# Performance work log

Hardware: AMD Instinct MI355X
Metric: run time of the kernel (lower is better)

## Reference

```python
import jax, jax.numpy as jnp
import numpy as np

B, S, D, H = 512, 256, 512, 512  # batch, seq_len, input_size, hidden_size (D==H required by module math)


def setup_inputs() -> dict:
    key = jax.random.key(0)
    ks = jax.random.split(key, 16)
    stdv = 1.0 / np.sqrt(H)
    u = lambda k, shp: jax.random.uniform(k, shp, jnp.float32, -stdv, stdv)
    return {
        "x": jax.random.normal(ks[0], (B, S, D), jnp.float32),
        "time_sen_seqs": jax.random.uniform(ks[1], (B, S), jnp.float32),  # attenuation rates in [0,1)
        "W_e": u(ks[2], (D, H)), "b_e": u(ks[3], (H,)),
        "U_i": u(ks[4], (D, H)), "V_i": u(ks[5], (H, H)), "b_i": u(ks[6], (H,)),
        "U_f": u(ks[7], (D, H)), "V_f": u(ks[8], (H, H)), "b_f": u(ks[9], (H,)),
        "U_c": u(ks[10], (D, H)), "V_c": u(ks[11], (H, H)), "b_c": u(ks[12], (H,)),
        "U_o": u(ks[13], (D, H)), "V_o": u(ks[14], (H, H)), "b_o": u(ks[15], (H,)),
    }


def reference(x, time_sen_seqs, W_e, b_e, U_i, V_i, b_i, U_f, V_f, b_f,
              U_c, V_c, b_c, U_o, V_o, b_o):
    bs = x.shape[0]
    h0 = jnp.zeros((bs, H), x.dtype)
    c0 = jnp.zeros((bs, H), x.dtype)

    # Precompute all input projections in one batched GEMM: [S, B, 4H]
    U = jnp.concatenate([U_i, U_f, U_c, U_o], axis=1)           # [D, 4H]
    b = jnp.concatenate([b_i, b_f, b_c, b_o], axis=0)           # [4H]
    x_proj = jnp.einsum('bsd,dk->sbk', x, U) + b                # [S, B, 4H]
    forget_seq = time_sen_seqs.T[..., None]                     # [S, B, 1]

    def step(carry, inp):
        h, c = carry
        xp, f_att = inp
        xi, xf, xc, xo = jnp.split(xp, 4, axis=-1)
        i_t = jax.nn.sigmoid(xi + h @ V_i)
        f_t = jax.nn.sigmoid(xf + h @ V_f)
        g_t = jnp.tanh(xc + h @ V_c)
        o_t = jax.nn.sigmoid(xo + h @ V_o)
        c = jnp.tanh((c * f_att) @ W_e + b_e)   # sentiment attenuation transform
        c = f_t * c + i_t * g_t
        h = o_t * jnp.tanh(c)
        return (h, c), h

    (h_t, c_t), hs = jax.lax.scan(step, (h0, c0), (x_proj, forget_seq))
    hidden_seq = hs.transpose(1, 0, 2)          # [B, S, H]
    return hidden_seq, (h_t, c_t)
```

## Files before the change

kernel.cpp:

```cpp
#include <hip/hip_runtime.h>

#define B_SZ 512
#define S_SZ 256
#define D_SZ 512
#define H_SZ 512

typedef __bf16 bf16x8 __attribute__((ext_vector_type(8)));
typedef __bf16 bf16x4 __attribute__((ext_vector_type(4)));
typedef float f32x4 __attribute__((ext_vector_type(4)));
typedef int i32x4 __attribute__((ext_vector_type(4)));
typedef unsigned long long u64;

#define FLAGS_BYTES 65536
#define STATE_OFF FLAGS_BYTES
#define STATE_PAR_ELEMS (2 * H_SZ * B_SZ)
#define GWT_OFF_BYTES (STATE_OFF + 2097152)
#define WET_OFF_BYTES (GWT_OFF_BYTES + 4194304)
#define XB_OFF_BYTES (WET_OFF_BYTES + 524288)
#define XB_BYTES ((size_t)B_SZ * S_SZ * D_SZ * 2)

#define SWZ(j, k) ((k) ^ (((j) & 7) << 3) ^ ((((j) >> 3) & 1) << 6))

__device__ __forceinline__ float sigmoidf_(float v) {
    return 1.f / (1.f + __expf(-v));
}
__device__ __forceinline__ float tanhf_(float v) {
    return 1.f - 2.f / (1.f + __expf(2.f * v));
}

__device__ __forceinline__ u64 coh_load(const u64* p) {
    return __hip_atomic_load(p, __ATOMIC_RELAXED, __HIP_MEMORY_SCOPE_AGENT);
}
__device__ __forceinline__ void coh_store(u64* p, u64 v) {
    __hip_atomic_store(p, v, __ATOMIC_RELAXED, __HIP_MEMORY_SCOPE_AGENT);
}

__global__ __launch_bounds__(256) void prep_weights(
    const float* __restrict__ We,
    const float* __restrict__ Ui, const float* __restrict__ Vi,
    const float* __restrict__ Uf, const float* __restrict__ Vf,
    const float* __restrict__ Uc, const float* __restrict__ Vc,
    const float* __restrict__ Uo, const float* __restrict__ Vo,
    __bf16* __restrict__ GwT, __bf16* __restrict__ WeT)
{
    const int bid = blockIdx.x;
    const int tid = threadIdx.x;
    if (bid < 2048) {
        const int g = bid >> 9;
        const int j = bid & 511;
        const float* U = (g == 0) ? Ui : (g == 1) ? Uf : (g == 2) ? Uc : Uo;
        const float* V = (g == 0) ? Vi : (g == 1) ? Vf : (g == 2) ? Vc : Vo;
        __bf16* dst = GwT + ((size_t)(g * 512 + j) << 10);
        for (int k = tid; k < 1024; k += 256) {
            float v = (k < 512) ? U[k * 512 + j] : V[(k - 512) * 512 + j];
            dst[k] = (__bf16)v;
        }
    } else {
        const int j = bid - 2048;
        __bf16* dst = WeT + ((size_t)j << 9);
        for (int k = tid; k < 512; k += 256) {
            dst[k] = (__bf16)We[k * 512 + j];
        }
    }
}

__global__ __launch_bounds__(256) void xcvt(const float* __restrict__ x,
                                            __bf16* __restrict__ xb)
{
    const size_t i = ((size_t)blockIdx.x * 256 + threadIdx.x) * 8;
    f32x4 a = *(const f32x4*)(x + i);
    f32x4 b = *(const f32x4*)(x + i + 4);
    bf16x8 o;
    o[0] = (__bf16)a[0]; o[1] = (__bf16)a[1]; o[2] = (__bf16)a[2]; o[3] = (__bf16)a[3];
    o[4] = (__bf16)b[0]; o[5] = (__bf16)b[1]; o[6] = (__bf16)b[2]; o[7] = (__bf16)b[3];
    *(bf16x8*)(xb + i) = o;
}

template <bool XB>
__global__ __launch_bounds__(256, 1) void lstm_persist(
    const float* __restrict__ x, const __bf16* __restrict__ xb,
    const float* __restrict__ tseq,
    const float* __restrict__ b_i, const float* __restrict__ b_f,
    const float* __restrict__ b_c, const float* __restrict__ b_o,
    const float* __restrict__ b_e,
    const __bf16* __restrict__ GwT, const __bf16* __restrict__ WeT,
    __bf16* __restrict__ state, int* __restrict__ flags,
    float* __restrict__ out)
{
    __shared__ __align__(16) __bf16 wlds[4][16][1024];
    __shared__ __align__(16) __bf16 welds[16][512];

    const int tid = threadIdx.x;
    const int bid = blockIdx.x;
    const int rblk = bid & 7;
    const int cblk = bid >> 3;
    const int j0 = cblk << 4;
    const int wave = tid >> 6;
    const int lane = tid & 63;
    const int alr = lane & 15;
    const int hq = lane >> 4;
    const int kbase = hq * 8;

    for (int e = tid * 8; e < 4 * 16 * 1024; e += 256 * 8) {
        const int g = e >> 14;
        const int j = (e >> 10) & 15;
        const int k = e & 1023;
        *(uint4*)&wlds[g][j][SWZ(j, k)] =
            *(const uint4*)&GwT[((size_t)(g * 512 + j0 + j) << 10) + k];
    }
    for (int e = tid * 8; e < 16 * 512; e += 256 * 8) {
        const int j = e >> 9;
        const int k = e & 511;
        *(uint4*)&welds[j][SWZ(j, k)] =
            *(const uint4*)&WeT[((size_t)(j0 + j) << 9) + k];
    }
    __syncthreads();

    bf16x8 wxr[8][4];
    #pragma unroll
    for (int kk = 0; kk < 8; ++kk)
        #pragma unroll
        for (int g = 0; g < 4; ++g)
            wxr[kk][g] = *(const bf16x8*)&wlds[g][alr][SWZ(alr, kk * 32 + kbase)];

    const int brow = rblk * 64 + wave * 16 + alr;
    const int jbase = j0 + hq * 4;
    const f32x4 Bi4 = *(const f32x4*)(b_i + jbase);
    const f32x4 Bf4 = *(const f32x4*)(b_f + jbase);
    const f32x4 Bc4 = *(const f32x4*)(b_c + jbase);
    const f32x4 Bo4 = *(const f32x4*)(b_o + jbase);
    const f32x4 Be4 = *(const f32x4*)(b_e + jbase);

    const float* xrow = x + (size_t)brow * S_SZ * D_SZ;
    const __bf16* xrowb = XB ? xb + (size_t)brow * S_SZ * D_SZ : nullptr;
    const float* tsrow = tseq + (size_t)brow * S_SZ;
    const size_t hoff = (size_t)brow * H_SZ;
    float* outrow = out + (size_t)brow * S_SZ * H_SZ + jbase;

    int* gflags = flags + rblk * 32 * 32;
    int* myflag = gflags + cblk * 32;
    const int* pollp = gflags + (lane & 31) * 32;

    int* xgrp = flags + 8192 + rblk * 32 * 32;
    unsigned xcc;
    asm volatile("s_getreg_b32 %0, hwreg(HW_REG_XCC_ID)" : "=s"(xcc));
    if (tid == 0)
        __hip_atomic_store(xgrp + cblk * 32, (int)xcc + 1,
                           __ATOMIC_RELAXED, __HIP_MEMORY_SCOPE_AGENT);
    int vx;
    const int* xpoll = xgrp + (lane & 31) * 32;
    for (;;) {
        vx = __hip_atomic_load(xpoll, __ATOMIC_RELAXED, __HIP_MEMORY_SCOPE_AGENT);
        if (__all(vx != 0)) break;
        __builtin_amdgcn_s_sleep(1);
    }
    const bool l2ok = __all(vx == __shfl(vx, 0, 64));

    bf16x8 xbf[16];
    if constexpr (XB) {
        #pragma unroll
        for (int kk = 0; kk < 16; ++kk)
            xbf[kk] = *(const bf16x8*)(xrowb + kk * 32 + kbase);
    } else {
        f32x4 xf0[32];
        #pragma unroll
        for (int kk = 0; kk < 16; ++kk) {
            xf0[2 * kk]     = *(const f32x4*)(xrow + kk * 32 + kbase);
            xf0[2 * kk + 1] = *(const f32x4*)(xrow + kk * 32 + kbase + 4);
        }
        #pragma unroll
        for (int kk = 0; kk < 16; ++kk) {
            f32x4 u = xf0[2 * kk], v = xf0[2 * kk + 1];
            bf16x8 a;
            a[0] = (__bf16)u[0]; a[1] = (__bf16)u[1]; a[2] = (__bf16)u[2]; a[3] = (__bf16)u[3];
            a[4] = (__bf16)v[0]; a[5] = (__bf16)v[1]; a[6] = (__bf16)v[2]; a[7] = (__bf16)v[3];
            xbf[kk] = a;
        }
    }

    for (int t = 0; t < S_SZ; ++t) {
        const __bf16* hp = state + (size_t)(t & 1) * STATE_PAR_ELEMS;
        const __bf16* cp = hp + (size_t)H_SZ * B_SZ;
        __bf16* hnx = state + (size_t)((t + 1) & 1) * STATE_PAR_ELEMS;
        __bf16* cnx = hnx + (size_t)H_SZ * B_SZ;

        const float fa = (t + 1 < S_SZ) ? tsrow[t + 1] : 0.f;
        union HU { i32x4 q; u64 u[2]; bf16x8 v; };
        HU hs[16], cs[16];
        if (l2ok) {
            const __bf16* hb = hp + hoff + kbase;
            const __bf16* cb = cp + hoff + kbase;
            #pragma unroll
            for (int kk = 0; kk < 16; ++kk) {
                hs[kk].q = *(const i32x4*)(hb + kk * 32);
                cs[kk].q = *(const i32x4*)(cb + kk * 32);
            }
        } else {
            #pragma unroll
            for (int kk = 0; kk < 16; ++kk) {
                const u64* ph = (const u64*)(hp + hoff + kbase + kk * 32);
                const u64* pc = (const u64*)(cp + hoff + kbase + kk * 32);
                hs[kk].u[0] = coh_load(ph);
                hs[kk].u[1] = coh_load(ph + 1);
                cs[kk].u[0] = coh_load(pc);
                cs[kk].u[1] = coh_load(pc + 1);
            }
        }

        f32x4 a0 = Bi4, a1 = Bf4, a2 = Bc4, a3 = Bo4, a4 = Be4;

        #pragma unroll
        for (int kk = 0; kk < 16; ++kk) {
            bf16x8 w0, w1, w2, w3;
            if (kk < 8) {
                w0 = wxr[kk][0]; w1 = wxr[kk][1]; w2 = wxr[kk][2]; w3 = wxr[kk][3];
            } else {
                const int k = SWZ(alr, kk * 32 + kbase);
                w0 = *(const bf16x8*)&wlds[0][alr][k];
                w1 = *(const bf16x8*)&wlds[1][alr][k];
                w2 = *(const bf16x8*)&wlds[2][alr][k];
                w3 = *(const bf16x8*)&wlds[3][alr][k];
            }
            a0 = __builtin_amdgcn_mfma_f32_16x16x32_bf16(w0, xbf[kk], a0, 0, 0, 0);
            a1 = __builtin_amdgcn_mfma_f32_16x16x32_bf16(w1, xbf[kk], a1, 0, 0, 0);
            a2 = __builtin_amdgcn_mfma_f32_16x16x32_bf16(w2, xbf[kk], a2, 0, 0, 0);
            a3 = __builtin_amdgcn_mfma_f32_16x16x32_bf16(w3, xbf[kk], a3, 0, 0, 0);
        }

        #pragma unroll
        for (int kk = 0; kk < 16; ++kk) {
            const int k = SWZ(alr, 512 + kk * 32 + kbase);
            bf16x8 w0 = *(const bf16x8*)&wlds[0][alr][k];
            bf16x8 w1 = *(const bf16x8*)&wlds[1][alr][k];
            bf16x8 w2 = *(const bf16x8*)&wlds[2][alr][k];
            bf16x8 w3 = *(const bf16x8*)&wlds[3][alr][k];
            bf16x8 we = *(const bf16x8*)&welds[alr][SWZ(alr, kk * 32 + kbase)];
            a0 = __builtin_amdgcn_mfma_f32_16x16x32_bf16(w0, hs[kk].v, a0, 0, 0, 0);
            a1 = __builtin_amdgcn_mfma_f32_16x16x32_bf16(w1, hs[kk].v, a1, 0, 0, 0);
            a2 = __builtin_amdgcn_mfma_f32_16x16x32_bf16(w2, hs[kk].v, a2, 0, 0, 0);
            a3 = __builtin_amdgcn_mfma_f32_16x16x32_bf16(w3, hs[kk].v, a3, 0, 0, 0);
            a4 = __builtin_amdgcn_mfma_f32_16x16x32_bf16(we, cs[kk].v, a4, 0, 0, 0);
        }

        const int tp = (t + 1 < S_SZ) ? t + 1 : t;
        f32x4 xf[32];
        if constexpr (XB) {
            const __bf16* xpn = xrowb + (size_t)tp * D_SZ;
            #pragma unroll
            for (int kk = 0; kk < 16; ++kk)
                xbf[kk] = *(const bf16x8*)(xpn + kk * 32 + kbase);
        } else {
            const float* xpn = xrow + (size_t)tp * D_SZ;
            #pragma unroll
            for (int kk = 0; kk < 16; ++kk) {
                xf[2 * kk]     = *(const f32x4*)(xpn + kk * 32 + kbase);
                xf[2 * kk + 1] = *(const f32x4*)(xpn + kk * 32 + kbase + 4);
            }
        }

        f32x4 hv4, cv4;
        union { bf16x4 v; u64 u; } ph8, pc8;
        #pragma unroll
        for (int e = 0; e < 4; ++e) {
            float it = sigmoidf_(a0[e]);
            float ft = sigmoidf_(a1[e]);
            float gt = tanhf_(a2[e]);
            float ot = sigmoidf_(a3[e]);
            float ctl = tanhf_(a4[e]);
            float cv = ft * ctl + it * gt;
            float hv = ot * tanhf_(cv);
            hv4[e] = hv; cv4[e] = cv;
            ph8.v[e] = (__bf16)hv;
            pc8.v[e] = (__bf16)(cv * fa);
        }
        __builtin_nontemporal_store(hv4, (f32x4*)(outrow + (size_t)t * H_SZ));
        if (t == S_SZ - 1) {
            float* tail = out + (size_t)B_SZ * S_SZ * H_SZ;
            *(f32x4*)(tail + hoff + jbase) = hv4;
            *(f32x4*)(tail + (size_t)B_SZ * H_SZ + hoff + jbase) = cv4;
        }

        if constexpr (!XB) {
            #pragma unroll
            for (int kk = 0; kk < 16; ++kk) {
                f32x4 u = xf[2 * kk], v = xf[2 * kk + 1];
                bf16x8 a;
                a[0] = (__bf16)u[0]; a[1] = (__bf16)u[1]; a[2] = (__bf16)u[2]; a[3] = (__bf16)u[3];
                a[4] = (__bf16)v[0]; a[5] = (__bf16)v[1]; a[6] = (__bf16)v[2]; a[7] = (__bf16)v[3];
                xbf[kk] = a;
            }
        }

        if (l2ok) {
            *(u64*)(hnx + hoff + jbase) = ph8.u;
            *(u64*)(cnx + hoff + jbase) = pc8.u;
        } else {
            coh_store((u64*)(hnx + hoff + jbase), ph8.u);
            coh_store((u64*)(cnx + hoff + jbase), pc8.u);
        }

        if (t < S_SZ - 1) {
            __syncthreads();
            if (tid == 0)
                __hip_atomic_store(myflag, t + 1, __ATOMIC_RELAXED,
                                   __HIP_MEMORY_SCOPE_AGENT);
            const int target = t + 1;
            for (;;) {
                int v = __hip_atomic_load(pollp, __ATOMIC_RELAXED,
                                          __HIP_MEMORY_SCOPE_AGENT);
                if (__all(v >= target)) break;
                __builtin_amdgcn_s_sleep(2);
            }
            if (l2ok)
                asm volatile("buffer_inv sc0" ::: "memory");
            __builtin_amdgcn_sched_barrier(0);
        }
    }
}

extern "C" void kernel_launch(void* const* d_in, const int* in_sizes, int n_in,
                              void* d_out, int out_size, void* d_ws, size_t ws_size,
                              hipStream_t stream) {
    const float* x  = (const float*)d_in[0];
    const float* ts = (const float*)d_in[1];
    const float* We = (const float*)d_in[2];
    const float* be = (const float*)d_in[3];
    const float* Ui = (const float*)d_in[4];
    const float* Vi = (const float*)d_in[5];
    const float* bi = (const float*)d_in[6];
    const float* Uf = (const float*)d_in[7];
    const float* Vf = (const float*)d_in[8];
    const float* bf = (const float*)d_in[9];
    const float* Uc = (const float*)d_in[10];
    const float* Vc = (const float*)d_in[11];
    const float* bc = (const float*)d_in[12];
    const float* Uo = (const float*)d_in[13];
    const float* Vo = (const float*)d_in[14];
    const float* bo = (const float*)d_in[15];

    char* ws = (char*)d_ws;
    int* flags = (int*)ws;
    __bf16* state = (__bf16*)(ws + STATE_OFF);
    __bf16* GwT = (__bf16*)(ws + GWT_OFF_BYTES);
    __bf16* WeT = (__bf16*)(ws + WET_OFF_BYTES);

    hipMemsetAsync(ws, 0, FLAGS_BYTES + 1048576, stream);
    prep_weights<<<2560, 256, 0, stream>>>(We, Ui, Vi, Uf, Vf, Uc, Vc, Uo, Vo, GwT, WeT);

    if (ws_size >= (size_t)XB_OFF_BYTES + XB_BYTES) {
        __bf16* xb = (__bf16*)(ws + XB_OFF_BYTES);
        xcvt<<<(int)(B_SZ * S_SZ * D_SZ / 8 / 256), 256, 0, stream>>>(x, xb);
        lstm_persist<true><<<256, 256, 0, stream>>>(x, xb, ts, bi, bf, bc, bo, be,
                                                    GwT, WeT, state, flags,
                                                    (float*)d_out);
    } else {
        lstm_persist<false><<<256, 256, 0, stream>>>(x, nullptr, ts, bi, bf, bc, bo,
                                                     be, GwT, WeT, state, flags,
                                                     (float*)d_out);
    }
}
```

Baseline: 1.858 ms.

## Split persistent LSTM block into input-projection and recurrent wave groups

Doubles the block to 512 threads. Four waves compute the x·U input projection and prefetch next-step x, while the other four load h/c, run the recurrent V and W_e MFMAs, and apply the gate activations. The partial input-projection sums are handed over through an LDS reduction buffer with an extra __syncthreads each step. The intent is to take the input-projection work off the serial critical path. In exchange it drops the register-cached weights, adds an LDS round trip and a barrier per step, and shortens the poll sleep.

```diff
diff --git a/kernel.cpp b/kernel.cpp
--- a/kernel.cpp
+++ b/kernel.cpp
@@ -77,7 +77,7 @@
 }
 
 template <bool XB>
-__global__ __launch_bounds__(256, 1) void lstm_persist(
+__global__ __launch_bounds__(512, 1) void lstm_persist(
     const float* __restrict__ x, const __bf16* __restrict__ xb,
     const float* __restrict__ tseq,
     const float* __restrict__ b_i, const float* __restrict__ b_f,
@@ -89,6 +89,7 @@
 {
     __shared__ __align__(16) __bf16 wlds[4][16][1024];
     __shared__ __align__(16) __bf16 welds[16][512];
+    __shared__ __align__(16) float red[4][64][16];
 
     const int tid = threadIdx.x;
     const int bid = blockIdx.x;
@@ -96,19 +97,21 @@
     const int cblk = bid >> 3;
     const int j0 = cblk << 4;
     const int wave = tid >> 6;
+    const int side = wave >> 2;
+    const int wrow = wave & 3;
     const int lane = tid & 63;
     const int alr = lane & 15;
     const int hq = lane >> 4;
     const int kbase = hq * 8;
 
-    for (int e = tid * 8; e < 4 * 16 * 1024; e += 256 * 8) {
+    for (int e = tid * 8; e < 4 * 16 * 1024; e += 512 * 8) {
         const int g = e >> 14;
         const int j = (e >> 10) & 15;
         const int k = e & 1023;
         *(uint4*)&wlds[g][j][SWZ(j, k)] =
             *(const uint4*)&GwT[((size_t)(g * 512 + j0 + j) << 10) + k];
     }
-    for (int e = tid * 8; e < 16 * 512; e += 256 * 8) {
+    for (int e = tid * 8; e < 16 * 512; e += 512 * 8) {
         const int j = e >> 9;
         const int k = e & 511;
         *(uint4*)&welds[j][SWZ(j, k)] =
@@ -116,14 +119,7 @@
     }
     __syncthreads();
 
-    bf16x8 wxr[8][4];
-    #pragma unroll
-    for (int kk = 0; kk < 8; ++kk)
-        #pragma unroll
-        for (int g = 0; g < 4; ++g)
-            wxr[kk][g] = *(const bf16x8*)&wlds[g][alr][SWZ(alr, kk * 32 + kbase)];
-
-    const int brow = rblk * 64 + wave * 16 + alr;
+    const int brow = rblk * 64 + wrow * 16 + alr;
     const int jbase = j0 + hq * 4;
     const f32x4 Bi4 = *(const f32x4*)(b_i + jbase);
     const f32x4 Bf4 = *(const f32x4*)(b_f + jbase);
@@ -157,24 +153,21 @@
     const bool l2ok = __all(vx == __shfl(vx, 0, 64));
 
     bf16x8 xbf[16];
-    if constexpr (XB) {
-        #pragma unroll
-        for (int kk = 0; kk < 16; ++kk)
-            xbf[kk] = *(const bf16x8*)(xrowb + kk * 32 + kbase);
-    } else {
-        f32x4 xf0[32];
-        #pragma unroll
-        for (int kk = 0; kk < 16; ++kk) {
-            xf0[2 * kk]     = *(const f32x4*)(xrow + kk * 32 + kbase);
-            xf0[2 * kk + 1] = *(const f32x4*)(xrow + kk * 32 + kbase + 4);
-        }
-        #pragma unroll
-        for (int kk = 0; kk < 16; ++kk) {
-            f32x4 u = xf0[2 * kk], v = xf0[2 * kk + 1];
-            bf16x8 a;
-            a[0] = (__bf16)u[0]; a[1] = (__bf16)u[1]; a[2] = (__bf16)u[2]; a[3] = (__bf16)u[3];
-            a[4] = (__bf16)v[0]; a[5] = (__bf16)v[1]; a[6] = (__bf16)v[2]; a[7] = (__bf16)v[3];
-            xbf[kk] = a;
+    if (side == 0) {
+        if constexpr (XB) {
+            #pragma unroll
+            for (int kk = 0; kk < 16; ++kk)
+                xbf[kk] = *(const bf16x8*)(xrowb + kk * 32 + kbase);
+        } else {
+            #pragma unroll
+            for (int kk = 0; kk < 16; ++kk) {
+                f32x4 u = *(const f32x4*)(xrow + kk * 32 + kbase);
+                f32x4 v = *(const f32x4*)(xrow + kk * 32 + kbase + 4);
+                bf16x8 a;
+                a[0] = (__bf16)u[0]; a[1] = (__bf16)u[1]; a[2] = (__bf16)u[2]; a[3] = (__bf16)u[3];
+                a[4] = (__bf16)v[0]; a[5] = (__bf16)v[1]; a[6] = (__bf16)v[2]; a[7] = (__bf16)v[3];
+                xbf[kk] = a;
+            }
         }
     }
 
@@ -184,119 +177,123 @@
         __bf16* hnx = state + (size_t)((t + 1) & 1) * STATE_PAR_ELEMS;
         __bf16* cnx = hnx + (size_t)H_SZ * B_SZ;
 
-        const float fa = (t + 1 < S_SZ) ? tsrow[t + 1] : 0.f;
+        f32x4 a0, a1, a2, a3, a4;
         union HU { i32x4 q; u64 u[2]; bf16x8 v; };
         HU hs[16], cs[16];
-        if (l2ok) {
-            const __bf16* hb = hp + hoff + kbase;
-            const __bf16* cb = cp + hoff + kbase;
+
+        if (side == 0) {
+            f32x4 p0 = {0,0,0,0}, p1 = {0,0,0,0}, p2 = {0,0,0,0}, p3 = {0,0,0,0};
             #pragma unroll
             for (int kk = 0; kk < 16; ++kk) {
-                hs[kk].q = *(const i32x4*)(hb + kk * 32);
-                cs[kk].q = *(const i32x4*)(cb + kk * 32);
-            }
+                const int k = SWZ(alr, kk * 32 + kbase);
+                bf16x8 w0 = *(const bf16x8*)&wlds[0][alr][k];
+                bf16x8 w1 = *(const bf16x8*)&wlds[1][alr][k];
+                bf16x8 w2 = *(const bf16x8*)&wlds[2][alr][k];
+                bf16x8 w3 = *(const bf16x8*)&wlds[3][alr][k];
+                p0 = __builtin_amdgcn_mfma_f32_16x16x32_bf16(w0, xbf[kk], p0, 0, 0, 0);
+                p1 = __builtin_amdgcn_mfma_f32_16x16x32_bf16(w1, xbf[kk], p1, 0, 0, 0);
+                p2 = __builtin_amdgcn_mfma_f32_16x16x32_bf16(w2, xbf[kk], p2, 0, 0, 0);
+                p3 = __builtin_amdgcn_mfma_f32_16x16x32_bf16(w3, xbf[kk], p3, 0, 0, 0);
+            }
+            float* rp = &red[wrow][lane][0];
+            *(f32x4*)(rp + 0)  = p0;
+            *(f32x4*)(rp + 4)  = p1;
+            *(f32x4*)(rp + 8)  = p2;
+            *(f32x4*)(rp + 12) = p3;
         } else {
+            if (l2ok) {
+                const __bf16* hb = hp + hoff + kbase;
+                const __bf16* cb = cp + hoff + kbase;
+                #pragma unroll
+                for (int kk = 0; kk < 16; ++kk) {
+                    hs[kk].q = *(const i32x4*)(hb + kk * 32);
+                    cs[kk].q = *(const i32x4*)(cb + kk * 32);
+                }
+            } else {
+                #pragma unroll
+                for (int kk = 0; kk < 16; ++kk) {
+                    const u64* ph = (const u64*)(hp + hoff + kbase + kk * 32);
+                    const u64* pc = (const u64*)(cp + hoff + kbase + kk * 32);
+                    hs[kk].u[0] = coh_load(ph);
+                    hs[kk].u[1] = coh_load(ph + 1);
+                    cs[kk].u[0] = coh_load(pc);
+                    cs[kk].u[1] = coh_load(pc + 1);
+                }
+            }
+            a0 = Bi4; a1 = Bf4; a2 = Bc4; a3 = Bo4; a4 = Be4;
             #pragma unroll
             for (int kk = 0; kk < 16; ++kk) {
-                const u64* ph = (const u64*)(hp + hoff + kbase + kk * 32);
-                const u64* pc = (const u64*)(cp + hoff + kbase + kk * 32);
-                hs[kk].u[0] = coh_load(ph);
-                hs[kk].u[1] = coh_load(ph + 1);
-                cs[kk].u[0] = coh_load(pc);
-                cs[kk].u[1] = coh_load(pc + 1);
-            }
-        }
-
-        f32x4 a0 = Bi4, a1 = Bf4, a2 = Bc4, a3 = Bo4, a4 = Be4;
-
-        #pragma unroll
-        for (int kk = 0; kk < 16; ++kk) {
-            bf16x8 w0, w1, w2, w3;
-            if (kk < 8) {
-                w0 = wxr[kk][0]; w1 = wxr[kk][1]; w2 = wxr[kk][2]; w3 = wxr[kk][3];
+                const int k = SWZ(alr, 512 + kk * 32 + kbase);
+                bf16x8 w0 = *(const bf16x8*)&wlds[0][alr][k];
+                bf16x8 w1 = *(const bf16x8*)&wlds[1][alr][k];
+                bf16x8 w2 = *(const bf16x8*)&wlds[2][alr][k];
+                bf16x8 w3 = *(const bf16x8*)&wlds[3][alr][k];
+                bf16x8 we = *(const bf16x8*)&welds[alr][SWZ(alr, kk * 32 + kbase)];
+                a0 = __builtin_amdgcn_mfma_f32_16x16x32_bf16(w0, hs[kk].v, a0, 0, 0, 0);
+                a1 = __builtin_amdgcn_mfma_f32_16x16x32_bf16(w1, hs[kk].v, a1, 0, 0, 0);
+                a2 = __builtin_amdgcn_mfma_f32_16x16x32_bf16(w2, hs[kk].v, a2, 0, 0, 0);
+                a3 = __builtin_amdgcn_mfma_f32_16x16x32_bf16(w3, hs[kk].v, a3, 0, 0, 0);
+                a4 = __builtin_amdgcn_mfma_f32_16x16x32_bf16(we, cs[kk].v, a4, 0, 0, 0);
+            }
+        }
+
+        __syncthreads();
+
+        if (side == 1) {
+            const float* rp = &red[wrow][lane][0];
+            a0 += *(const f32x4*)(rp + 0);
+            a1 += *(const f32x4*)(rp + 4);
+            a2 += *(const f32x4*)(rp + 8);
+            a3 += *(const f32x4*)(rp + 12);
+
+            const float fa = (t + 1 < S_SZ) ? tsrow[t + 1] : 0.f;
+            f32x4 hv4, cv4;
+            union { bf16x4 v; u64 u; } ph8, pc8;
+            #pragma unroll
+            for (int e = 0; e < 4; ++e) {
+                float it = sigmoidf_(a0[e]);
+                float ft = sigmoidf_(a1[e]);
+                float gt = tanhf_(a2[e]);
+                float ot = sigmoidf_(a3[e]);
+                float ctl = tanhf_(a4[e]);
+                float cv = ft * ctl + it * gt;
+                float hv = ot * tanhf_(cv);
+                hv4[e] = hv; cv4[e] = cv;
+                ph8.v[e] = (__bf16)hv;
+                pc8.v[e] = (__bf16)(cv * fa);
+            }
+            __builtin_nontemporal_store(hv4, (f32x4*)(outrow + (size_t)t * H_SZ));
+            if (t == S_SZ - 1) {
+                float* tail = out + (size_t)B_SZ * S_SZ * H_SZ;
+                *(f32x4*)(tail + hoff + jbase) = hv4;
+                *(f32x4*)(tail + (size_t)B_SZ * H_SZ + hoff + jbase) = cv4;
+            }
+            if (l2ok) {
+                *(u64*)(hnx + hoff + jbase) = ph8.u;
+                *(u64*)(cnx + hoff + jbase) = pc8.u;
             } else {
-                const int k = SWZ(alr, kk * 32 + kbase);
-                w0 = *(const bf16x8*)&wlds[0][alr][k];
-                w1 = *(const bf16x8*)&wlds[1][alr][k];
-                w2 = *(const bf16x8*)&wlds[2][alr][k];
-                w3 = *(const bf16x8*)&wlds[3][alr][k];
-            }
-            a0 = __builtin_amdgcn_mfma_f32_16x16x32_bf16(w0, xbf[kk], a0, 0, 0, 0);
-            a1 = __builtin_amdgcn_mfma_f32_16x16x32_bf16(w1, xbf[kk], a1, 0, 0, 0);
-            a2 = __builtin_amdgcn_mfma_f32_16x16x32_bf16(w2, xbf[kk], a2, 0, 0, 0);
-            a3 = __builtin_amdgcn_mfma_f32_16x16x32_bf16(w3, xbf[kk], a3, 0, 0, 0);
-        }
-
-        #pragma unroll
-        for (int kk = 0; kk < 16; ++kk) {
-            const int k = SWZ(alr, 512 + kk * 32 + kbase);
-            bf16x8 w0 = *(const bf16x8*)&wlds[0][alr][k];
-            bf16x8 w1 = *(const bf16x8*)&wlds[1][alr][k];
-            bf16x8 w2 = *(const bf16x8*)&wlds[2][alr][k];
-            bf16x8 w3 = *(const bf16x8*)&wlds[3][alr][k];
-            bf16x8 we = *(const bf16x8*)&welds[alr][SWZ(alr, kk * 32 + kbase)];
-            a0 = __builtin_amdgcn_mfma_f32_16x16x32_bf16(w0, hs[kk].v, a0, 0, 0, 0);
-            a1 = __builtin_amdgcn_mfma_f32_16x16x32_bf16(w1, hs[kk].v, a1, 0, 0, 0);
-            a2 = __builtin_amdgcn_mfma_f32_16x16x32_bf16(w2, hs[kk].v, a2, 0, 0, 0);
-            a3 = __builtin_amdgcn_mfma_f32_16x16x32_bf16(w3, hs[kk].v, a3, 0, 0, 0);
-            a4 = __builtin_amdgcn_mfma_f32_16x16x32_bf16(we, cs[kk].v, a4, 0, 0, 0);
-        }
-
-        const int tp = (t + 1 < S_SZ) ? t + 1 : t;
-        f32x4 xf[32];
-        if constexpr (XB) {
-            const __bf16* xpn = xrowb + (size_t)tp * D_SZ;
-            #pragma unroll
-            for (int kk = 0; kk < 16; ++kk)
-                xbf[kk] = *(const bf16x8*)(xpn + kk * 32 + kbase);
+                coh_store((u64*)(hnx + hoff + jbase), ph8.u);
+                coh_store((u64*)(cnx + hoff + jbase), pc8.u);
+            }
         } else {
-            const float* xpn = xrow + (size_t)tp * D_SZ;
-            #pragma unroll
-            for (int kk = 0; kk < 16; ++kk) {
-                xf[2 * kk]     = *(const f32x4*)(xpn + kk * 32 + kbase);
-                xf[2 * kk + 1] = *(const f32x4*)(xpn + kk * 32 + kbase + 4);
-            }
-        }
-
-        f32x4 hv4, cv4;
-        union { bf16x4 v; u64 u; } ph8, pc8;
-        #pragma unroll
-        for (int e = 0; e < 4; ++e) {
-            float it = sigmoidf_(a0[e]);
-            float ft = sigmoidf_(a1[e]);
-            float gt = tanhf_(a2[e]);
-            float ot = sigmoidf_(a3[e]);
-            float ctl = tanhf_(a4[e]);
-            float cv = ft * ctl + it * gt;
-            float hv = ot * tanhf_(cv);
-            hv4[e] = hv; cv4[e] = cv;
-            ph8.v[e] = (__bf16)hv;
-            pc8.v[e] = (__bf16)(cv * fa);
-        }
-        __builtin_nontemporal_store(hv4, (f32x4*)(outrow + (size_t)t * H_SZ));
-        if (t == S_SZ - 1) {
-            float* tail = out + (size_t)B_SZ * S_SZ * H_SZ;
-            *(f32x4*)(tail + hoff + jbase) = hv4;
-            *(f32x4*)(tail + (size_t)B_SZ * H_SZ + hoff + jbase) = cv4;
-        }
-
-        if constexpr (!XB) {
-            #pragma unroll
-            for (int kk = 0; kk < 16; ++kk) {
-                f32x4 u = xf[2 * kk], v = xf[2 * kk + 1];
-                bf16x8 a;
-                a[0] = (__bf16)u[0]; a[1] = (__bf16)u[1]; a[2] = (__bf16)u[2]; a[3] = (__bf16)u[3];
-                a[4] = (__bf16)v[0]; a[5] = (__bf16)v[1]; a[6] = (__bf16)v[2]; a[7] = (__bf16)v[3];
-                xbf[kk] = a;
-            }
-        }
-
-        if (l2ok) {
-            *(u64*)(hnx + hoff + jbase) = ph8.u;
-            *(u64*)(cnx + hoff + jbase) = pc8.u;
-        } else {
-            coh_store((u64*)(hnx + hoff + jbase), ph8.u);
-            coh_store((u64*)(cnx + hoff + jbase), pc8.u);
+            const int tp = (t + 1 < S_SZ) ? t + 1 : t;
+            if constexpr (XB) {
+                const __bf16* xpn = xrowb + (size_t)tp * D_SZ;
+                #pragma unroll
+                for (int kk = 0; kk < 16; ++kk)
+                    xbf[kk] = *(const bf16x8*)(xpn + kk * 32 + kbase);
+            } else {
+                const float* xpn = xrow + (size_t)tp * D_SZ;
+                #pragma unroll
+                for (int kk = 0; kk < 16; ++kk) {
+                    f32x4 u = *(const f32x4*)(xpn + kk * 32 + kbase);
+                    f32x4 v = *(const f32x4*)(xpn + kk * 32 + kbase + 4);
+                    bf16x8 a;
+                    a[0] = (__bf16)u[0]; a[1] = (__bf16)u[1]; a[2] = (__bf16)u[2]; a[3] = (__bf16)u[3];
+                    a[4] = (__bf16)v[0]; a[5] = (__bf16)v[1]; a[6] = (__bf16)v[2]; a[7] = (__bf16)v[3];
+                    xbf[kk] = a;
+                }
+            }
         }
 
         if (t < S_SZ - 1) {
@@ -309,7 +306,7 @@
                 int v = __hip_atomic_load(pollp, __ATOMIC_RELAXED,
                                           __HIP_MEMORY_SCOPE_AGENT);
                 if (__all(v >= target)) break;
-                __builtin_amdgcn_s_sleep(2);
+                __builtin_amdgcn_s_sleep(1);
             }
             if (l2ok)
                 asm volatile("buffer_inv sc0" ::: "memory");
@@ -350,11 +347,11 @@
     if (ws_size >= (size_t)XB_OFF_BYTES + XB_BYTES) {
         __bf16* xb = (__bf16*)(ws + XB_OFF_BYTES);
         xcvt<<<(int)(B_SZ * S_SZ * D_SZ / 8 / 256), 256, 0, stream>>>(x, xb);
-        lstm_persist<true><<<256, 256, 0, stream>>>(x, xb, ts, bi, bf, bc, bo, be,
+        lstm_persist<true><<<256, 512, 0, stream>>>(x, xb, ts, bi, bf, bc, bo, be,
                                                     GwT, WeT, state, flags,
                                                     (float*)d_out);
     } else {
-        lstm_persist<false><<<256, 256, 0, stream>>>(x, nullptr, ts, bi, bf, bc, bo,
+        lstm_persist<false><<<256, 512, 0, stream>>>(x, nullptr, ts, bi, bf, bc, bo,
                                                      be, GwT, WeT, state, flags,
                                                      (float*)d_out);
     }
```

Measured after the change: 5.107 ms. 175% more time.

## Add 512-block persistent LSTM variant with 8-column tiles and pipelined state loads

Applied to the files above, without the earlier changes.

Adds a second persistent kernel that splits the hidden dimension into 8-column tiles across 512 blocks (two per CU via launch bounds), halving per-block LDS weights. It chunks the h/c state loads into double-buffered groups of four, interleaved with the MFMA consumption. The host picks this variant when the occupancy query reports two resident blocks per CU, otherwise it falls back to the old kernel. The goal is more parallelism per recurrent step and hiding state-load latency. The cost is that each step's barrier must now sync 64 blocks per row group instead of 32, and half the lanes do redundant MFMA work on padded columns.

```diff
diff --git a/kernel.cpp b/kernel.cpp
--- a/kernel.cpp
+++ b/kernel.cpp
@@ -11,7 +11,9 @@
 typedef int i32x4 __attribute__((ext_vector_type(4)));
 typedef unsigned long long u64;
 
-#define FLAGS_BYTES 65536
+#define FLAGS_BYTES 131072
+#define GRPI 2048
+#define XCCI 16384
 #define STATE_OFF FLAGS_BYTES
 #define STATE_PAR_ELEMS (2 * H_SZ * B_SZ)
 #define GWT_OFF_BYTES (STATE_OFF + 2097152)
@@ -76,8 +78,24 @@
     *(bf16x8*)(xb + i) = o;
 }
 
+union HU { i32x4 q; u64 u[2]; bf16x8 v; };
+
+#define LD16(dst, basep, kkidx) do {                                          \
+    if (l2ok) { (dst).q = *(const i32x4*)((basep) + (kkidx) * 32); }          \
+    else { const u64* _p = (const u64*)((basep) + (kkidx) * 32);              \
+           (dst).u[0] = coh_load(_p); (dst).u[1] = coh_load(_p + 1); }        \
+} while (0)
+
+#define LOADCH(hbuf, cbuf, kk0) do {                                          \
+    _Pragma("unroll")                                                         \
+    for (int i_ = 0; i_ < 4; ++i_) {                                          \
+        LD16((hbuf)[i_], hb, (kk0) + i_);                                     \
+        LD16((cbuf)[i_], cb, (kk0) + i_);                                     \
+    }                                                                         \
+} while (0)
+
 template <bool XB>
-__global__ __launch_bounds__(256, 1) void lstm_persist(
+__global__ __launch_bounds__(256, 1) void lstm_v1(
     const float* __restrict__ x, const __bf16* __restrict__ xb,
     const float* __restrict__ tseq,
     const float* __restrict__ b_i, const float* __restrict__ b_f,
@@ -137,11 +155,11 @@
     const size_t hoff = (size_t)brow * H_SZ;
     float* outrow = out + (size_t)brow * S_SZ * H_SZ + jbase;
 
-    int* gflags = flags + rblk * 32 * 32;
+    int* gflags = flags + rblk * GRPI;
     int* myflag = gflags + cblk * 32;
     const int* pollp = gflags + (lane & 31) * 32;
 
-    int* xgrp = flags + 8192 + rblk * 32 * 32;
+    int* xgrp = flags + XCCI + rblk * GRPI;
     unsigned xcc;
     asm volatile("s_getreg_b32 %0, hwreg(HW_REG_XCC_ID)" : "=s"(xcc));
     if (tid == 0)
@@ -162,15 +180,10 @@
         for (int kk = 0; kk < 16; ++kk)
             xbf[kk] = *(const bf16x8*)(xrowb + kk * 32 + kbase);
     } else {
-        f32x4 xf0[32];
         #pragma unroll
         for (int kk = 0; kk < 16; ++kk) {
-            xf0[2 * kk]     = *(const f32x4*)(xrow + kk * 32 + kbase);
-            xf0[2 * kk + 1] = *(const f32x4*)(xrow + kk * 32 + kbase + 4);
-        }
-        #pragma unroll
-        for (int kk = 0; kk < 16; ++kk) {
-            f32x4 u = xf0[2 * kk], v = xf0[2 * kk + 1];
+            f32x4 u = *(const f32x4*)(xrow + kk * 32 + kbase);
+            f32x4 v = *(const f32x4*)(xrow + kk * 32 + kbase + 4);
             bf16x8 a;
             a[0] = (__bf16)u[0]; a[1] = (__bf16)u[1]; a[2] = (__bf16)u[2]; a[3] = (__bf16)u[3];
             a[4] = (__bf16)v[0]; a[5] = (__bf16)v[1]; a[6] = (__bf16)v[2]; a[7] = (__bf16)v[3];
@@ -185,7 +198,6 @@
         __bf16* cnx = hnx + (size_t)H_SZ * B_SZ;
 
         const float fa = (t + 1 < S_SZ) ? tsrow[t + 1] : 0.f;
-        union HU { i32x4 q; u64 u[2]; bf16x8 v; };
         HU hs[16], cs[16];
         if (l2ok) {
             const __bf16* hb = hp + hoff + kbase;
@@ -297,6 +309,229 @@
         } else {
             coh_store((u64*)(hnx + hoff + jbase), ph8.u);
             coh_store((u64*)(cnx + hoff + jbase), pc8.u);
+        }
+
+        if (t < S_SZ - 1) {
+            __syncthreads();
+            if (tid == 0)
+                __hip_atomic_store(myflag, t + 1, __ATOMIC_RELAXED,
+                                   __HIP_MEMORY_SCOPE_AGENT);
+            const int target = t + 1;
+            for (;;) {
+                int v = __hip_atomic_load(pollp, __ATOMIC_RELAXED,
+                                          __HIP_MEMORY_SCOPE_AGENT);
+                if (__all(v >= target)) break;
+                __builtin_amdgcn_s_sleep(2);
+            }
+            if (l2ok)
+                asm volatile("buffer_inv sc0" ::: "memory");
+            __builtin_amdgcn_sched_barrier(0);
+        }
+    }
+}
+
+template <bool XB>
+__global__ __launch_bounds__(256, 2) void lstm_v2(
+    const float* __restrict__ x, const __bf16* __restrict__ xb,
+    const float* __restrict__ tseq,
+    const float* __restrict__ b_i, const float* __restrict__ b_f,
+    const float* __restrict__ b_c, const float* __restrict__ b_o,
+    const float* __restrict__ b_e,
+    const __bf16* __restrict__ GwT, const __bf16* __restrict__ WeT,
+    __bf16* __restrict__ state, int* __restrict__ flags,
+    float* __restrict__ out)
+{
+    __shared__ __align__(16) __bf16 wlds[4][8][1024];
+    __shared__ __align__(16) __bf16 welds[8][512];
+
+    const int tid = threadIdx.x;
+    const int bid = blockIdx.x;
+    const int rblk = bid & 7;
+    const int cblk = bid >> 3;
+    const int j0 = cblk << 3;
+    const int wave = tid >> 6;
+    const int lane = tid & 63;
+    const int alr = lane & 15;
+    const int aj = alr & 7;
+    const int hq = lane >> 4;
+    const int kbase = hq * 8;
+    const bool jval = hq < 2;
+
+    for (int e = tid * 8; e < 4 * 8 * 1024; e += 256 * 8) {
+        const int g = e >> 13;
+        const int j = (e >> 10) & 7;
+        const int k = e & 1023;
+        *(uint4*)&wlds[g][j][SWZ(j, k)] =
+            *(const uint4*)&GwT[((size_t)(g * 512 + j0 + j) << 10) + k];
+    }
+    for (int e = tid * 8; e < 8 * 512; e += 256 * 8) {
+        const int j = e >> 9;
+        const int k = e & 511;
+        *(uint4*)&welds[j][SWZ(j, k)] =
+            *(const uint4*)&WeT[((size_t)(j0 + j) << 9) + k];
+    }
+    __syncthreads();
+
+    const int brow = rblk * 64 + wave * 16 + alr;
+    const int jbase = j0 + (hq & 1) * 4;
+    const f32x4 Bi4 = *(const f32x4*)(b_i + jbase);
+    const f32x4 Bf4 = *(const f32x4*)(b_f + jbase);
+    const f32x4 Bc4 = *(const f32x4*)(b_c + jbase);
+    const f32x4 Bo4 = *(const f32x4*)(b_o + jbase);
+    const f32x4 Be4 = *(const f32x4*)(b_e + jbase);
+
+    const float* xrow = x + (size_t)brow * S_SZ * D_SZ;
+    const __bf16* xrowb = XB ? xb + (size_t)brow * S_SZ * D_SZ : nullptr;
+    const float* tsrow = tseq + (size_t)brow * S_SZ;
+    const size_t hoff = (size_t)brow * H_SZ;
+    float* outrow = out + (size_t)brow * S_SZ * H_SZ + jbase;
+
+    int* gflags = flags + rblk * GRPI;
+    int* myflag = gflags + cblk * 32;
+    const int* pollp = gflags + lane * 32;
+
+    int* xgrp = flags + XCCI + rblk * GRPI;
+    unsigned xcc;
+    asm volatile("s_getreg_b32 %0, hwreg(HW_REG_XCC_ID)" : "=s"(xcc));
+    if (tid == 0)
+        __hip_atomic_store(xgrp + cblk * 32, (int)xcc + 1,
+                           __ATOMIC_RELAXED, __HIP_MEMORY_SCOPE_AGENT);
+    int vx;
+    const int* xpoll = xgrp + lane * 32;
+    for (;;) {
+        vx = __hip_atomic_load(xpoll, __ATOMIC_RELAXED, __HIP_MEMORY_SCOPE_AGENT);
+        if (__all(vx != 0)) break;
+        __builtin_amdgcn_s_sleep(1);
+    }
+    const bool l2ok = __all(vx == __shfl(vx, 0, 64));
+
+    bf16x8 xbf[16];
+    if constexpr (XB) {
+        #pragma unroll
+        for (int kk = 0; kk < 16; ++kk)
+            xbf[kk] = *(const bf16x8*)(xrowb + kk * 32 + kbase);
+    } else {
+        #pragma unroll
+        for (int kk = 0; kk < 16; ++kk) {
+            f32x4 u = *(const f32x4*)(xrow + kk * 32 + kbase);
+            f32x4 v = *(const f32x4*)(xrow + kk * 32 + kbase + 4);
+            bf16x8 a;
+            a[0] = (__bf16)u[0]; a[1] = (__bf16)u[1]; a[2] = (__bf16)u[2]; a[3] = (__bf16)u[3];
+            a[4] = (__bf16)v[0]; a[5] = (__bf16)v[1]; a[6] = (__bf16)v[2]; a[7] = (__bf16)v[3];
+            xbf[kk] = a;
+        }
+    }
+
+    for (int t = 0; t < S_SZ; ++t) {
+        const __bf16* hp = state + (size_t)(t & 1) * STATE_PAR_ELEMS;
+        const __bf16* cp = hp + (size_t)H_SZ * B_SZ;
+        __bf16* hnx = state + (size_t)((t + 1) & 1) * STATE_PAR_ELEMS;
+        __bf16* cnx = hnx + (size_t)H_SZ * B_SZ;
+
+        const float fa = (t + 1 < S_SZ) ? tsrow[t + 1] : 0.f;
+        const __bf16* hb = hp + hoff + kbase;
+        const __bf16* cb = cp + hoff + kbase;
+
+        HU hA[4], cA[4], hB[4], cB[4];
+        LOADCH(hA, cA, 0);
+        LOADCH(hB, cB, 4);
+
+        f32x4 a0 = Bi4, a1 = Bf4, a2 = Bc4, a3 = Bo4, a4 = Be4;
+
+        #pragma unroll
+        for (int kk = 0; kk < 16; ++kk) {
+            const int k = SWZ(aj, kk * 32 + kbase);
+            bf16x8 w0 = *(const bf16x8*)&wlds[0][aj][k];
+            bf16x8 w1 = *(const bf16x8*)&wlds[1][aj][k];
+            bf16x8 w2 = *(const bf16x8*)&wlds[2][aj][k];
+            bf16x8 w3 = *(const bf16x8*)&wlds[3][aj][k];
+            a0 = __builtin_amdgcn_mfma_f32_16x16x32_bf16(w0, xbf[kk], a0, 0, 0, 0);
+            a1 = __builtin_amdgcn_mfma_f32_16x16x32_bf16(w1, xbf[kk], a1, 0, 0, 0);
+            a2 = __builtin_amdgcn_mfma_f32_16x16x32_bf16(w2, xbf[kk], a2, 0, 0, 0);
+            a3 = __builtin_amdgcn_mfma_f32_16x16x32_bf16(w3, xbf[kk], a3, 0, 0, 0);
+        }
+
+        #define CONS(hbuf, cbuf, kk0) do {                                    \
+            _Pragma("unroll")                                                 \
+            for (int i_ = 0; i_ < 4; ++i_) {                                  \
+                const int kk_ = (kk0) + i_;                                   \
+                const int k_ = SWZ(aj, 512 + kk_ * 32 + kbase);               \
+                bf16x8 w0 = *(const bf16x8*)&wlds[0][aj][k_];                 \
+                bf16x8 w1 = *(const bf16x8*)&wlds[1][aj][k_];                 \
+                bf16x8 w2 = *(const bf16x8*)&wlds[2][aj][k_];                 \
+                bf16x8 w3 = *(const bf16x8*)&wlds[3][aj][k_];                 \
+                bf16x8 we = *(const bf16x8*)&welds[aj][SWZ(aj, kk_ * 32 + kbase)]; \
+                a0 = __builtin_amdgcn_mfma_f32_16x16x32_bf16(w0, (hbuf)[i_].v, a0, 0, 0, 0); \
+                a1 = __builtin_amdgcn_mfma_f32_16x16x32_bf16(w1, (hbuf)[i_].v, a1, 0, 0, 0); \
+                a2 = __builtin_amdgcn_mfma_f32_16x16x32_bf16(w2, (hbuf)[i_].v, a2, 0, 0, 0); \
+                a3 = __builtin_amdgcn_mfma_f32_16x16x32_bf16(w3, (hbuf)[i_].v, a3, 0, 0, 0); \
+                a4 = __builtin_amdgcn_mfma_f32_16x16x32_bf16(we, (cbuf)[i_].v, a4, 0, 0, 0); \
+            }                                                                 \
+        } while (0)
+        CONS(hA, cA, 0);
+        LOADCH(hA, cA, 8);
+        CONS(hB, cB, 4);
+        LOADCH(hB, cB, 12);
+        CONS(hA, cA, 8);
+        CONS(hB, cB, 12);
+        #undef CONS
+
+        const int tp = (t + 1 < S_SZ) ? t + 1 : t;
+        f32x4 xf[32];
+        if constexpr (XB) {
+            const __bf16* xpn = xrowb + (size_t)tp * D_SZ;
+            #pragma unroll
+            for (int kk = 0; kk < 16; ++kk)
+                xbf[kk] = *(const bf16x8*)(xpn + kk * 32 + kbase);
+        } else {
+            const float* xpn = xrow + (size_t)tp * D_SZ;
+            #pragma unroll
+            for (int kk = 0; kk < 16; ++kk) {
+                xf[2 * kk]     = *(const f32x4*)(xpn + kk * 32 + kbase);
+                xf[2 * kk + 1] = *(const f32x4*)(xpn + kk * 32 + kbase + 4);
+            }
+        }
+
+        f32x4 hv4, cv4;
+        union { bf16x4 v; u64 u; } ph8, pc8;
+        #pragma unroll
+        for (int e = 0; e < 4; ++e) {
+            float it = sigmoidf_(a0[e]);
+            float ft = sigmoidf_(a1[e]);
+            float gt = tanhf_(a2[e]);
+            float ot = sigmoidf_(a3[e]);
+            float ctl = tanhf_(a4[e]);
+            float cv = ft * ctl + it * gt;
+            float hv = ot * tanhf_(cv);
+            hv4[e] = hv; cv4[e] = cv;
+            ph8.v[e] = (__bf16)hv;
+            pc8.v[e] = (__bf16)(cv * fa);
+        }
+        if (jval) {
+            __builtin_nontemporal_store(hv4, (f32x4*)(outrow + (size_t)t * H_SZ));
+            if (t == S_SZ - 1) {
+                float* tail = out + (size_t)B_SZ * S_SZ * H_SZ;
+                *(f32x4*)(tail + hoff + jbase) = hv4;
+                *(f32x4*)(tail + (size_t)B_SZ * H_SZ + hoff + jbase) = cv4;
+            }
+            if (l2ok) {
+                *(u64*)(hnx + hoff + jbase) = ph8.u;
+                *(u64*)(cnx + hoff + jbase) = pc8.u;
+            } else {
+                coh_store((u64*)(hnx + hoff + jbase), ph8.u);
+                coh_store((u64*)(cnx + hoff + jbase), pc8.u);
+            }
+        }
+
+        if constexpr (!XB) {
+            #pragma unroll
+            for (int kk = 0; kk < 16; ++kk) {
+                f32x4 u = xf[2 * kk], v = xf[2 * kk + 1];
+                bf16x8 a;
+                a[0] = (__bf16)u[0]; a[1] = (__bf16)u[1]; a[2] = (__bf16)u[2]; a[3] = (__bf16)u[3];
+                a[4] = (__bf16)v[0]; a[5] = (__bf16)v[1]; a[6] = (__bf16)v[2]; a[7] = (__bf16)v[3];
+                xbf[kk] = a;
+            }
         }
 
         if (t < S_SZ - 1) {
@@ -347,15 +582,36 @@
     hipMemsetAsync(ws, 0, FLAGS_BYTES + 1048576, stream);
     prep_weights<<<2560, 256, 0, stream>>>(We, Ui, Vi, Uf, Vf, Uc, Vc, Uo, Vo, GwT, WeT);
 
-    if (ws_size >= (size_t)XB_OFF_BYTES + XB_BYTES) {
-        __bf16* xb = (__bf16*)(ws + XB_OFF_BYTES);
-        xcvt<<<(int)(B_SZ * S_SZ * D_SZ / 8 / 256), 256, 0, stream>>>(x, xb);
-        lstm_persist<true><<<256, 256, 0, stream>>>(x, xb, ts, bi, bf, bc, bo, be,
-                                                    GwT, WeT, state, flags,
+    const bool xbok = ws_size >= (size_t)XB_OFF_BYTES + XB_BYTES;
+    __bf16* xbp = (__bf16*)(ws + XB_OFF_BYTES);
+    if (xbok)
+        xcvt<<<(int)(B_SZ * S_SZ * D_SZ / 8 / 256), 256, 0, stream>>>(x, xbp);
+
+    int nb = 0;
+    if (xbok)
+        hipOccupancyMaxActiveBlocksPerMultiprocessor(
+            &nb, reinterpret_cast<const void*>(&lstm_v2<true>), 256, 0);
+    else
+        hipOccupancyMaxActiveBlocksPerMultiprocessor(
+            &nb, reinterpret_cast<const void*>(&lstm_v2<false>), 256, 0);
+
+    if (nb >= 2) {
+        if (xbok)
+            lstm_v2<true><<<512, 256, 0, stream>>>(x, xbp, ts, bi, bf, bc, bo, be,
+                                                   GwT, WeT, state, flags,
+                                                   (float*)d_out);
+        else
+            lstm_v2<false><<<512, 256, 0, stream>>>(x, nullptr, ts, bi, bf, bc, bo,
+                                                    be, GwT, WeT, state, flags,
                                                     (float*)d_out);
     } else {
-        lstm_persist<false><<<256, 256, 0, stream>>>(x, nullptr, ts, bi, bf, bc, bo,
-                                                     be, GwT, WeT, state, flags,
-                                                     (float*)d_out);
-    }
-}
+        if (xbok)
+            lstm_v1<true><<<256, 256, 0, stream>>>(x, xbp, ts, bi, bf, bc, bo, be,
+                                                   GwT, WeT, state, flags,
+                                                   (float*)d_out);
+        else
+            lstm_v1<false><<<256, 256, 0, stream>>>(x, nullptr, ts, bi, bf, bc, bo,
+                                                    be, GwT, WeT, state, flags,
+                                                    (float*)d_out);
+    }
+}
```

Result: no change. 1.861 ms (+0.1%).
